# Kernel tuning notes

Hardware: AMD Instinct MI355X
Metric: run time of the kernel (lower is better)

Reference implementation:

```python
import jax, jax.numpy as jnp
import numpy as np
from jax import lax

N, D, H = 4096, 768, 16384


def setup_inputs() -> dict:
    key = jax.random.key(0)
    k0, k1, k2, k3, k4, k5, k6 = jax.random.split(key, 7)
    bound_e = 1.0 / np.sqrt(D)   # kaiming_uniform(a=sqrt(5)) on (H, D) -> bound 1/sqrt(fan_in)
    bound_d = 1.0 / np.sqrt(H)   # nn.Linear default init, fan_in = H
    return {
        "vision_embeddings": jax.random.normal(k0, (N, D), dtype=jnp.float32),
        "text_embeddings": jax.random.normal(k1, (N, D), dtype=jnp.float32),
        "encoder": jax.random.uniform(k2, (H, D), jnp.float32, -bound_e, bound_e),
        "Wv": jax.random.uniform(k3, (D, H), jnp.float32, -bound_d, bound_d),
        "bv": jax.random.uniform(k4, (D,), jnp.float32, -bound_d, bound_d),
        "Wt": jax.random.uniform(k5, (D, H), jnp.float32, -bound_d, bound_d),
        "bt": jax.random.uniform(k6, (D,), jnp.float32, -bound_d, bound_d),
        "topk": 32,
    }


def _l2norm(x, axis):
    return x / jnp.maximum(jnp.linalg.norm(x, axis=axis, keepdims=True), 1e-12)


def _encode(emb, encoder, topk):
    # F.normalize rows, then cdist(p=2) between unit vectors: ||a-b|| = sqrt(2-2 a.b)
    w = _l2norm(encoder, axis=1)            # [H, D]
    e = _l2norm(emb, axis=1)                # [N, D]
    cos = jnp.einsum("nd,hd->nh", e, w)     # [N, H]
    dist = jnp.sqrt(jnp.maximum(2.0 - 2.0 * cos, 0.0))
    sim = 2.0 - dist                         # [N, H]
    # kthvalue(abs, k=H-topk) == (topk+1)-th largest; keep strictly-greater entries
    abs_f = jnp.abs(sim)
    thres = lax.top_k(abs_f, topk + 1)[0][:, -1]  # [N]
    mask = (abs_f > thres[:, None]).astype(sim.dtype)
    return sim * mask


def reference(vision_embeddings, text_embeddings, encoder, Wv, bv, Wt, bt, topk):
    latent_v = _encode(vision_embeddings, encoder, topk)          # [N, H]
    recon_v = jnp.einsum("nh,dh->nd", latent_v, Wv) + bv          # [N, D]
    latent_t = _encode(text_embeddings, encoder, topk)            # [N, H]
    recon_t = jnp.einsum("nh,dh->nd", latent_t, Wt) + bt          # [N, D]
    return (recon_v, recon_t, latent_v, latent_t)
```

## Files before the change

kernel.cpp:

```cpp
#include <hip/hip_runtime.h>
#include <math.h>


#define N_ROWS 4096
#define D_DIM  768
#define H_DIM  16384
#define M_TOT  8192
#define TOPK   32
#define MARGIN 1e-3f
#define SEL_CAP 40
#define AMB_CAP 64
#define CAP2   512

typedef __attribute__((ext_vector_type(8))) short short8;
typedef __attribute__((ext_vector_type(4))) float floatx4;

__device__ inline unsigned short bf16_rne(float f) {
    unsigned u = __float_as_uint(f);
    unsigned r = u + 0x7fffu + ((u >> 16) & 1u);
    return (unsigned short)(r >> 16);
}

__device__ inline void gload16(const unsigned short* g, unsigned short* l) {
    __builtin_amdgcn_global_load_lds(
        (const __attribute__((address_space(1))) void*)g,
        (__attribute__((address_space(3))) void*)l, 16, 0, 0);
}

__global__ void split_all_kernel(const float* __restrict__ embv,
                                 const float* __restrict__ embt,
                                 const float* __restrict__ enc,
                                 unsigned short* __restrict__ Ahi,
                                 unsigned short* __restrict__ Alo,
                                 unsigned short* __restrict__ Bh,
                                 float* __restrict__ invA,
                                 float* __restrict__ invB)
{
    int row = blockIdx.x;
    int tid = threadIdx.x;
    const float* src;
    unsigned short *hi, *lo;
    float* invp;
    if (row < N_ROWS) {
        src = embv + (size_t)row * D_DIM;
        hi = Ahi + (size_t)row * D_DIM; lo = Alo + (size_t)row * D_DIM;
        invp = invA + row;
    } else if (row < 2 * N_ROWS) {
        int r = row - N_ROWS;
        src = embt + (size_t)r * D_DIM;
        hi = Ahi + (size_t)row * D_DIM; lo = Alo + (size_t)row * D_DIM;
        invp = invA + row;
    } else {
        int r = row - 2 * N_ROWS;
        src = enc + (size_t)r * D_DIM;
        hi = Bh + (size_t)r * D_DIM; lo = nullptr;
        invp = invB + r;
    }
    __shared__ float red[4];
    const float4* s4 = reinterpret_cast<const float4*>(src);
    float4 v = make_float4(0.f, 0.f, 0.f, 0.f);
    float ss = 0.f;
    if (tid < 192) {
        v = s4[tid];
        ss = v.x * v.x + v.y * v.y + v.z * v.z + v.w * v.w;
    }
    #pragma unroll
    for (int o = 32; o > 0; o >>= 1) ss += __shfl_down(ss, o);
    int wave = tid >> 6, lane = tid & 63;
    if (lane == 0) red[wave] = ss;
    __syncthreads();
    if (tid == 0) {
        float tot = red[0] + red[1] + red[2];
        red[0] = 1.f / fmaxf(sqrtf(tot), 1e-12f);
    }
    __syncthreads();
    float inv = red[0];
    if (tid == 0) *invp = inv;
    if (tid < 192) {
        float x[4] = {v.x * inv, v.y * inv, v.z * inv, v.w * inv};
        unsigned short hh[4], ll[4];
        #pragma unroll
        for (int t = 0; t < 4; t++) {
            hh[t] = bf16_rne(x[t]);
            float hf = __uint_as_float((unsigned)hh[t] << 16);
            ll[t] = bf16_rne(x[t] - hf);
        }
        ushort4 h4; h4.x = hh[0]; h4.y = hh[1]; h4.z = hh[2]; h4.w = hh[3];
        *reinterpret_cast<ushort4*>(hi + tid * 4) = h4;
        if (lo) {
            ushort4 l4; l4.x = ll[0]; l4.y = ll[1]; l4.z = ll[2]; l4.w = ll[3];
            *reinterpret_cast<ushort4*>(lo + tid * 4) = l4;
        }
    }
}

#define GBK 32

__global__ __launch_bounds__(256, 4)
void gemm_mfma_kernel(const unsigned short* __restrict__ Ahi,
                      const unsigned short* __restrict__ Alo,
                      const unsigned short* __restrict__ Bh,
                      float* __restrict__ latent)
{
    __shared__ unsigned short sA[2][128 * GBK];
    __shared__ unsigned short sB[128 * GBK];

    int tid = threadIdx.x;
    int lane = tid & 63;
    int wave = tid >> 6;
    int wr = (wave >> 1) * 64;
    int wc = (wave & 1) * 64;
    int m = lane & 15;
    int q = lane >> 4;

    int row0 = blockIdx.y * 128;
    int col0 = blockIdx.x * 128;

    int p0 = tid, p1 = tid + 256;
    int r0 = ((p0 >> 5) << 3) | (p0 & 7), q0 = (p0 >> 3) & 3;
    int r1 = ((p1 >> 5) << 3) | (p1 & 7), q1 = (p1 >> 3) & 3;
    size_t aoff0 = (size_t)(row0 + r0) * D_DIM + q0 * 8;
    size_t aoff1 = (size_t)(row0 + r1) * D_DIM + q1 * 8;
    size_t boff0 = (size_t)(col0 + r0) * D_DIM + q0 * 8;
    size_t boff1 = (size_t)(col0 + r1) * D_DIM + q1 * 8;

    int am0 = wr + m;
    int bn0 = wc + m;
    int offA = ((am0 >> 3) << 8) + (q << 6) + ((am0 & 7) << 3);
    int offB = ((bn0 >> 3) << 8) + (q << 6) + ((bn0 & 7) << 3);

    floatx4 acc[4][4];
    #pragma unroll
    for (int i = 0; i < 4; i++)
        #pragma unroll
        for (int j = 0; j < 4; j++)
            acc[i][j] = (floatx4){0.f, 0.f, 0.f, 0.f};

    for (int k0 = 0; k0 < D_DIM; k0 += GBK) {
        gload16(Ahi + aoff0 + k0, &sA[0][p0 * 8]);
        gload16(Ahi + aoff1 + k0, &sA[0][p1 * 8]);
        gload16(Alo + aoff0 + k0, &sA[1][p0 * 8]);
        gload16(Alo + aoff1 + k0, &sA[1][p1 * 8]);
        gload16(Bh + boff0 + k0, &sB[p0 * 8]);
        gload16(Bh + boff1 + k0, &sB[p1 * 8]);
        __syncthreads();

        short8 fah[4], fal[4];
        #pragma unroll
        for (int i = 0; i < 4; i++) {
            fah[i] = *(const short8*)&sA[0][offA + i * 512];
            fal[i] = *(const short8*)&sA[1][offA + i * 512];
        }
        #pragma unroll
        for (int j = 0; j < 4; j++) {
            short8 fb = *(const short8*)&sB[offB + j * 512];
            #pragma unroll
            for (int i = 0; i < 4; i++) {
                acc[i][j] = __builtin_amdgcn_mfma_f32_16x16x32_bf16(fah[i], fb, acc[i][j], 0, 0, 0);
                acc[i][j] = __builtin_amdgcn_mfma_f32_16x16x32_bf16(fal[i], fb, acc[i][j], 0, 0, 0);
            }
        }
        __syncthreads();
    }

    #pragma unroll
    for (int i = 0; i < 4; i++) {
        #pragma unroll
        for (int r = 0; r < 4; r++) {
            int grow = row0 + wr + i * 16 + q * 4 + r;
            float* dst = latent + (size_t)grow * H_DIM + col0 + wc + m;
            #pragma unroll
            for (int j = 0; j < 4; j++) {
                float cosv = acc[i][j][r];
                float sim = 2.f - sqrtf(fmaxf(2.f - 2.f * cosv, 0.f));
                dst[j * 16] = sim;
            }
        }
    }
}

__global__ __launch_bounds__(256)
void select_kernel(float* __restrict__ latent,
                   int* __restrict__ sel_cnt,
                   int* __restrict__ sel_idx,
                   float* __restrict__ sel_val,
                   int* __restrict__ amb_cnt,
                   int* __restrict__ amb_idx)
{
    int row = blockIdx.x;
    int tid = threadIdx.x;
    float* v = latent + (size_t)row * H_DIM;
    const float4* v4 = (const float4*)v;
    float4* vw = (float4*)v;

    __shared__ _Float16 hbuf[H_DIM];
    __shared__ float smax[256];
    __shared__ float sca[CAP2];
    __shared__ int   sci[CAP2];
    __shared__ float sT;
    __shared__ int scnt, svstar, skept, samb;

    float mx = -1.f;
    #pragma unroll 4
    for (int k = 0; k < 16; k++) {
        int i = tid + 256 * k;
        float4 x = v4[i];
        float a0 = fabsf(x.x), a1 = fabsf(x.y), a2 = fabsf(x.z), a3 = fabsf(x.w);
        hbuf[4 * i + 0] = (_Float16)a0;
        hbuf[4 * i + 1] = (_Float16)a1;
        hbuf[4 * i + 2] = (_Float16)a2;
        hbuf[4 * i + 3] = (_Float16)a3;
        mx = fmaxf(mx, fmaxf(fmaxf(a0, a1), fmaxf(a2, a3)));
    }
    smax[tid] = mx;
    if (tid == 0) { scnt = 0; svstar = 0x7FFFFFFF; skept = 0; samb = 0; }
    __syncthreads();

    int gt = 0;
    for (int j = 0; j < 256; j++) {
        float mj = smax[j];
        gt += (mj > mx || (mj == mx && j < tid)) ? 1 : 0;
    }
    if (gt == 32) sT = mx;
    __syncthreads();
    float Tm = sT - MARGIN;

    #pragma unroll 4
    for (int k = 0; k < 16; k++) {
        int i = tid + 256 * k;
        float a[4];
        a[0] = (float)hbuf[4 * i + 0]; a[1] = (float)hbuf[4 * i + 1];
        a[2] = (float)hbuf[4 * i + 2]; a[3] = (float)hbuf[4 * i + 3];
        bool any = (a[0] >= Tm) | (a[1] >= Tm) | (a[2] >= Tm) | (a[3] >= Tm);
        if (any) {
            #pragma unroll
            for (int t = 0; t < 4; t++) {
                if (a[t] >= Tm) {
                    int c = atomicAdd(&scnt, 1);
                    if (c < CAP2) { sci[c] = 4 * i + t; sca[c] = v[4 * i + t]; }
                }
            }
        }
        vw[i] = make_float4(0.f, 0.f, 0.f, 0.f);
    }
    __syncthreads();

    int C = min(scnt, CAP2);
    for (int c = tid; c < C; c += 256) {
        float a = fabsf(sca[c]);
        int g = 0;
        for (int j = 0; j < C; j++) {
            float aj = fabsf(sca[j]);
            g += (aj > a || (aj == a && j < c)) ? 1 : 0;
        }
        if (g <= TOPK) atomicMin(&svstar, __float_as_int(a));
    }
    __syncthreads();
    float vs = __int_as_float(svstar);

    for (int c = tid; c < C; c += 256) {
        float f = sca[c];
        float a = fabsf(f);
        int idx = sci[c];
        if (a > vs + MARGIN) {
            int s = atomicAdd(&skept, 1);
            sel_idx[(size_t)row * SEL_CAP + s] = idx;
            sel_val[(size_t)row * SEL_CAP + s] = f;
            v[idx] = f;
        } else if (a >= vs - MARGIN) {
            int s = atomicAdd(&samb, 1);
            if (s < AMB_CAP) amb_idx[(size_t)row * AMB_CAP + s] = idx;
        }
    }
    __syncthreads();
    if (tid == 0) { sel_cnt[row] = skept; amb_cnt[row] = min(samb, AMB_CAP); }
}

__global__ void refine_kernel(const float* __restrict__ embv,
                              const float* __restrict__ embt,
                              const float* __restrict__ enc,
                              const float* __restrict__ invA,
                              const float* __restrict__ invB,
                              float* __restrict__ latent,
                              int* __restrict__ sel_cnt,
                              int* __restrict__ sel_idx,
                              float* __restrict__ sel_val,
                              const int* __restrict__ amb_cnt,
                              const int* __restrict__ amb_idx)
{
    int row = blockIdx.x;
    int s = amb_cnt[row];
    if (s == 0) return;
    int tid = threadIdx.x;
    int m = sel_cnt[row];
    int need = TOPK - m;
    float* v = latent + (size_t)row * H_DIM;
    if (need <= 0) return;
    __shared__ float ex[AMB_CAP];
    __shared__ int evs, kc;
    const float* src = (row < N_ROWS) ? embv + (size_t)row * D_DIM
                                      : embt + (size_t)(row - N_ROWS) * D_DIM;
    float ia = invA[row];
    int wave = tid >> 6, lane = tid & 63;
    for (int a = wave; a < s; a += 4) {
        int h = amb_idx[(size_t)row * AMB_CAP + a];
        const float* w = enc + (size_t)h * D_DIM;
        float d = 0.f;
        for (int t = lane; t < D_DIM; t += 64) d += src[t] * w[t];
        #pragma unroll
        for (int o = 32; o > 0; o >>= 1) d += __shfl_down(d, o);
        if (lane == 0) {
            float cosv = d * ia * invB[h];
            ex[a] = 2.f - sqrtf(fmaxf(2.f - 2.f * cosv, 0.f));
        }
    }
    if (tid == 0) { evs = 0x7FFFFFFF; kc = 0; }
    __syncthreads();
    if (tid < s) {
        float mya = fabsf(ex[tid]);
        int g = 0;
        for (int j = 0; j < s; j++) {
            float aj = fabsf(ex[j]);
            g += (aj > mya || (aj == mya && j < tid)) ? 1 : 0;
        }
        if (g <= need) atomicMin(&evs, __float_as_int(mya));
    }
    __syncthreads();
    float ep = __int_as_float(evs);
    if (tid < s) {
        int idx = amb_idx[(size_t)row * AMB_CAP + tid];
        float e = ex[tid];
        if (fabsf(e) > ep) {
            int sl = atomicAdd(&kc, 1);
            v[idx] = e;
            sel_idx[(size_t)row * SEL_CAP + m + sl] = idx;
            sel_val[(size_t)row * SEL_CAP + m + sl] = e;
        }
    }
    __syncthreads();
    if (tid == 0) sel_cnt[row] = m + kc;
}

__global__ void transpose_kernel(const float* __restrict__ Wv,
                                 const float* __restrict__ Wt,
                                 float* __restrict__ WvT,
                                 float* __restrict__ WtT)
{
    int z = blockIdx.z;
    const float* W = z ? Wt : Wv;
    float* WT = z ? WtT : WvT;
    __shared__ float tile[32][33];
    int tx = threadIdx.x & 31;
    int ty = threadIdx.x >> 5;
    int h0 = blockIdx.x * 32;
    int d0 = blockIdx.y * 32;
    #pragma unroll
    for (int t = 0; t < 4; t++)
        tile[ty + t * 8][tx] = W[(size_t)(d0 + ty + t * 8) * H_DIM + h0 + tx];
    __syncthreads();
    #pragma unroll
    for (int t = 0; t < 4; t++)
        WT[(size_t)(h0 + ty + t * 8) * D_DIM + d0 + tx] = tile[tx][ty + t * 8];
}

__global__ void recon_kernel(const float* __restrict__ Wv_,
                             const float* __restrict__ Wt_,
                             const float* __restrict__ bv,
                             const float* __restrict__ bt,
                             const int* __restrict__ sel_cnt,
                             const int* __restrict__ sel_idx,
                             const float* __restrict__ sel_val,
                             long sh, long sd,
                             float* __restrict__ out)
{
    int n = blockIdx.x;
    int z = blockIdx.y;
    int row = z * N_ROWS + n;
    const float* W = z ? Wt_ : Wv_;
    const float* bias = z ? bt : bv;
    float* o = out + (size_t)z * N_ROWS * D_DIM + (size_t)n * D_DIM;

    __shared__ int s_idx[SEL_CAP];
    __shared__ float s_val[SEL_CAP];
    __shared__ int s_cnt;
    int tid = threadIdx.x;
    if (tid == 0) s_cnt = sel_cnt[row];
    __syncthreads();
    int cnt = s_cnt;
    if (tid < cnt) {
        s_idx[tid] = sel_idx[(size_t)row * SEL_CAP + tid];
        s_val[tid] = sel_val[(size_t)row * SEL_CAP + tid];
    }
    __syncthreads();

    for (int d = tid; d < D_DIM; d += 256) {
        float acc = bias[d];
        for (int j = 0; j < cnt; j++)
            acc += s_val[j] * W[(size_t)s_idx[j] * sh + (size_t)d * sd];
        o[d] = acc;
    }
}

__global__ void row_invnorm_kernel(const float* __restrict__ x,
                                   float* __restrict__ inv, int rows) {
    int row = blockIdx.x * 4 + (threadIdx.x >> 6);
    int lane = threadIdx.x & 63;
    if (row >= rows) return;
    const float4* p = reinterpret_cast<const float4*>(x + (size_t)row * D_DIM);
    float ss = 0.f;
    #pragma unroll
    for (int i = 0; i < 3; i++) {
        float4 v = p[lane + i * 64];
        ss += v.x * v.x + v.y * v.y + v.z * v.z + v.w * v.w;
    }
    #pragma unroll
    for (int off = 32; off > 0; off >>= 1) ss += __shfl_down(ss, off);
    if (lane == 0) inv[row] = 1.f / fmaxf(sqrtf(ss), 1e-12f);
}

#define BM 128
#define BN 128
#define BK 16
__global__ __launch_bounds__(256)
void gemm_sim_kernel(const float* __restrict__ embv,
                     const float* __restrict__ embt,
                     const float* __restrict__ enc,
                     const float* __restrict__ inv_emb,
                     const float* __restrict__ inv_enc,
                     float* __restrict__ latent)
{
    int z = blockIdx.z;
    const float* A = z ? embt : embv;
    const float* invA = inv_emb + z * N_ROWS;
    float* C = latent + (size_t)z * N_ROWS * H_DIM;
    __shared__ float As[BK][BM + 4];
    __shared__ float Bs[BK][BN + 4];
    int tid = threadIdx.x;
    int tx = tid & 15, ty = tid >> 4;
    int row0 = blockIdx.y * BM, col0 = blockIdx.x * BN;
    float acc[8][8];
    #pragma unroll
    for (int i = 0; i < 8; i++)
        #pragma unroll
        for (int j = 0; j < 8; j++) acc[i][j] = 0.f;
    for (int k0 = 0; k0 < D_DIM; k0 += BK) {
        #pragma unroll
        for (int t = 0; t < 2; t++) {
            int idx = t * 256 + tid;
            int r = idx >> 2, c4 = idx & 3;
            float4 va = *reinterpret_cast<const float4*>(
                A + (size_t)(row0 + r) * D_DIM + k0 + c4 * 4);
            As[c4 * 4 + 0][r] = va.x; As[c4 * 4 + 1][r] = va.y;
            As[c4 * 4 + 2][r] = va.z; As[c4 * 4 + 3][r] = va.w;
            float4 vb = *reinterpret_cast<const float4*>(
                enc + (size_t)(col0 + r) * D_DIM + k0 + c4 * 4);
            Bs[c4 * 4 + 0][r] = vb.x; Bs[c4 * 4 + 1][r] = vb.y;
            Bs[c4 * 4 + 2][r] = vb.z; Bs[c4 * 4 + 3][r] = vb.w;
        }
        __syncthreads();
        #pragma unroll
        for (int kk = 0; kk < BK; kk++) {
            float a[8], b[8];
            *reinterpret_cast<float4*>(&a[0]) = *reinterpret_cast<const float4*>(&As[kk][ty * 8]);
            *reinterpret_cast<float4*>(&a[4]) = *reinterpret_cast<const float4*>(&As[kk][ty * 8 + 4]);
            *reinterpret_cast<float4*>(&b[0]) = *reinterpret_cast<const float4*>(&Bs[kk][tx * 8]);
            *reinterpret_cast<float4*>(&b[4]) = *reinterpret_cast<const float4*>(&Bs[kk][tx * 8 + 4]);
            #pragma unroll
            for (int i = 0; i < 8; i++)
                #pragma unroll
                for (int j = 0; j < 8; j++)
                    acc[i][j] = fmaf(a[i], b[j], acc[i][j]);
        }
        __syncthreads();
    }
    #pragma unroll
    for (int i = 0; i < 8; i++) {
        int n = row0 + ty * 8 + i;
        float sa = invA[n];
        float* Crow = C + (size_t)n * H_DIM + col0 + tx * 8;
        float tmp[8];
        #pragma unroll
        for (int j = 0; j < 8; j++) {
            float cosv = acc[i][j] * sa * inv_enc[col0 + tx * 8 + j];
            tmp[j] = 2.f - sqrtf(fmaxf(2.f - 2.f * cosv, 0.f));
        }
        float4 o0 = {tmp[0], tmp[1], tmp[2], tmp[3]};
        float4 o1 = {tmp[4], tmp[5], tmp[6], tmp[7]};
        *reinterpret_cast<float4*>(Crow) = o0;
        *reinterpret_cast<float4*>(Crow + 4) = o1;
    }
}

__global__ void legacy_select_kernel(float* __restrict__ latent,
                                     const int* __restrict__ topk_p,
                                     int* __restrict__ sel_cnt,
                                     int* __restrict__ sel_idx,
                                     float* __restrict__ sel_val)
{
    int row = blockIdx.x;
    float* v = latent + (size_t)row * H_DIM;
    int tid = threadIdx.x;
    __shared__ unsigned hist[256];
    __shared__ unsigned s_prefix;
    __shared__ int s_k;
    __shared__ int s_cnt;
    int k = topk_p[0] + 1;
    unsigned prefix = 0;
    for (int shift = 24; shift >= 0; shift -= 8) {
        hist[tid] = 0;
        __syncthreads();
        unsigned pmask = (shift == 24) ? 0u : (0xFFFFFFFFu << (shift + 8));
        for (int i = tid; i < H_DIM; i += 256) {
            unsigned u = __float_as_uint(v[i]) & 0x7FFFFFFFu;
            if ((u & pmask) == prefix)
                atomicAdd(&hist[(u >> shift) & 255u], 1u);
        }
        __syncthreads();
        if (tid == 0) {
            int c = 0, b = 255;
            for (; b >= 0; b--) {
                c += (int)hist[b];
                if (c >= k) break;
            }
            if (b < 0) b = 0;
            s_prefix = prefix | ((unsigned)b << shift);
            s_k = k - (c - (int)hist[b]);
        }
        __syncthreads();
        prefix = s_prefix;
        k = s_k;
        __syncthreads();
    }
    float thres = __uint_as_float(prefix);
    if (tid == 0) s_cnt = 0;
    __syncthreads();
    for (int i = tid; i < H_DIM; i += 256) {
        float x = v[i];
        bool keep = (fabsf(x) > thres);
        v[i] = keep ? x : 0.f;
        if (keep) {
            int slot = atomicAdd(&s_cnt, 1);
            if (slot < SEL_CAP) {
                sel_idx[(size_t)row * SEL_CAP + slot] = i;
                sel_val[(size_t)row * SEL_CAP + slot] = x;
            }
        }
    }
    __syncthreads();
    if (tid == 0) sel_cnt[row] = (s_cnt > SEL_CAP) ? SEL_CAP : s_cnt;
}

extern "C" void kernel_launch(void* const* d_in, const int* in_sizes, int n_in,
                              void* d_out, int out_size, void* d_ws, size_t ws_size,
                              hipStream_t stream) {
    const float* embv = (const float*)d_in[0];
    const float* embt = (const float*)d_in[1];
    const float* enc  = (const float*)d_in[2];
    const float* Wv   = (const float*)d_in[3];
    const float* bv   = (const float*)d_in[4];
    const float* Wt   = (const float*)d_in[5];
    const float* bt   = (const float*)d_in[6];
    const int* topk   = (const int*)d_in[7];
    float* out = (float*)d_out;

    float* recon_out = out;
    float* latent = out + (size_t)2 * N_ROWS * D_DIM;

    char* ws = (char*)d_ws;
    size_t off = 0;
    float* invA = (float*)(ws + off);            off += (size_t)M_TOT * 4;
    float* invB = (float*)(ws + off);            off += (size_t)H_DIM * 4;
    int*   sel_cnt = (int*)(ws + off);           off += (size_t)M_TOT * 4;
    int*   amb_cnt = (int*)(ws + off);           off += (size_t)M_TOT * 4;
    int*   sel_idx = (int*)(ws + off);           off += (size_t)M_TOT * SEL_CAP * 4;
    float* sel_val = (float*)(ws + off);         off += (size_t)M_TOT * SEL_CAP * 4;
    int*   amb_idx = (int*)(ws + off);           off += (size_t)M_TOT * AMB_CAP * 4;
    unsigned short* Ahi = (unsigned short*)(ws + off); off += (size_t)M_TOT * D_DIM * 2;
    unsigned short* Alo = (unsigned short*)(ws + off); off += (size_t)M_TOT * D_DIM * 2;
    unsigned short* Bh  = (unsigned short*)(ws + off); off += (size_t)H_DIM * D_DIM * 2;
    size_t core_need = off;
    float* WvT = (float*)(ws + off);
    float* WtT = WvT + (size_t)D_DIM * H_DIM;
    size_t full_need = off + (size_t)2 * D_DIM * H_DIM * 4;

    if (ws_size >= core_need) {
        bool use_T = ws_size >= full_need;

        split_all_kernel<<<2 * N_ROWS + H_DIM, 256, 0, stream>>>(
            embv, embt, enc, Ahi, Alo, Bh, invA, invB);

        gemm_mfma_kernel<<<dim3(H_DIM / 128, M_TOT / 128), 256, 0, stream>>>(
            Ahi, Alo, Bh, latent);

        select_kernel<<<M_TOT, 256, 0, stream>>>(latent,
            sel_cnt, sel_idx, sel_val, amb_cnt, amb_idx);

        refine_kernel<<<M_TOT, 256, 0, stream>>>(embv, embt, enc, invA, invB,
            latent, sel_cnt, sel_idx, sel_val, amb_cnt, amb_idx);

        if (use_T) {
            transpose_kernel<<<dim3(H_DIM / 32, D_DIM / 32, 2), 256, 0, stream>>>(
                Wv, Wt, WvT, WtT);
            recon_kernel<<<dim3(N_ROWS, 2), 256, 0, stream>>>(
                WvT, WtT, bv, bt, sel_cnt, sel_idx, sel_val, (long)D_DIM, 1L, recon_out);
        } else {
            recon_kernel<<<dim3(N_ROWS, 2), 256, 0, stream>>>(
                Wv, Wt, bv, bt, sel_cnt, sel_idx, sel_val, 1L, (long)H_DIM, recon_out);
        }
    } else {
        size_t o2 = 0;
        float* inv_enc = (float*)(ws + o2); o2 += (size_t)H_DIM * 4;
        float* inv_emb = (float*)(ws + o2); o2 += (size_t)2 * N_ROWS * 4;
        int*   l_cnt = (int*)(ws + o2);     o2 += (size_t)2 * N_ROWS * 4;
        int*   l_idx = (int*)(ws + o2);     o2 += (size_t)2 * N_ROWS * SEL_CAP * 4;
        float* l_val = (float*)(ws + o2);   o2 += (size_t)2 * N_ROWS * SEL_CAP * 4;
        row_invnorm_kernel<<<H_DIM / 4, 256, 0, stream>>>(enc, inv_enc, H_DIM);
        row_invnorm_kernel<<<N_ROWS / 4, 256, 0, stream>>>(embv, inv_emb, N_ROWS);
        row_invnorm_kernel<<<N_ROWS / 4, 256, 0, stream>>>(embt, inv_emb + N_ROWS, N_ROWS);
        dim3 g(H_DIM / BN, N_ROWS / BM, 2);
        gemm_sim_kernel<<<g, 256, 0, stream>>>(embv, embt, enc, inv_emb, inv_enc, latent);
        legacy_select_kernel<<<2 * N_ROWS, 256, 0, stream>>>(latent, topk, l_cnt, l_idx, l_val);
        recon_kernel<<<dim3(N_ROWS, 2), 256, 0, stream>>>(
            Wv, Wt, bv, bt, l_cnt, l_idx, l_val, 1L, (long)H_DIM, recon_out);
    }
}
```

Measured before the change: 1.723 ms.

## Double-buffer GEMM LDS tiles, swizzle workgroups, use nontemporal latent stores

```diff
diff --git a/kernel.cpp b/kernel.cpp
--- a/kernel.cpp
+++ b/kernel.cpp
@@ -95,15 +95,16 @@
 }
 
 #define GBK 32
-
-__global__ __launch_bounds__(256, 4)
+#define NTILE (D_DIM / GBK)
+
+__global__ __launch_bounds__(256, 3)
 void gemm_mfma_kernel(const unsigned short* __restrict__ Ahi,
                       const unsigned short* __restrict__ Alo,
                       const unsigned short* __restrict__ Bh,
                       float* __restrict__ latent)
 {
-    __shared__ unsigned short sA[2][128 * GBK];
-    __shared__ unsigned short sB[128 * GBK];
+    __shared__ unsigned short sA[2][2][128 * GBK];
+    __shared__ unsigned short sB[2][128 * GBK];
 
     int tid = threadIdx.x;
     int lane = tid & 63;
@@ -113,8 +114,15 @@
     int m = lane & 15;
     int q = lane >> 4;
 
-    int row0 = blockIdx.y * 128;
-    int col0 = blockIdx.x * 128;
+    unsigned nwgx = gridDim.x;
+    unsigned lid = blockIdx.y * nwgx + blockIdx.x;
+    unsigned cpx = (nwgx * gridDim.y) >> 3;
+    unsigned swz = (lid & 7u) * cpx + (lid >> 3);
+    int bx = (int)(swz % nwgx);
+    int by = (int)(swz / nwgx);
+
+    int row0 = by * 128;
+    int col0 = bx * 128;
 
     int p0 = tid, p1 = tid + 256;
     int r0 = ((p0 >> 5) << 3) | (p0 & 7), q0 = (p0 >> 3) & 3;
@@ -136,32 +144,54 @@
         for (int j = 0; j < 4; j++)
             acc[i][j] = (floatx4){0.f, 0.f, 0.f, 0.f};
 
-    for (int k0 = 0; k0 < D_DIM; k0 += GBK) {
-        gload16(Ahi + aoff0 + k0, &sA[0][p0 * 8]);
-        gload16(Ahi + aoff1 + k0, &sA[0][p1 * 8]);
-        gload16(Alo + aoff0 + k0, &sA[1][p0 * 8]);
-        gload16(Alo + aoff1 + k0, &sA[1][p1 * 8]);
-        gload16(Bh + boff0 + k0, &sB[p0 * 8]);
-        gload16(Bh + boff1 + k0, &sB[p1 * 8]);
-        __syncthreads();
-
-        short8 fah[4], fal[4];
+    auto stage = [&](int t, int b) {
+        int k0 = t * GBK;
+        gload16(Ahi + aoff0 + k0, &sA[b][0][p0 * 8]);
+        gload16(Ahi + aoff1 + k0, &sA[b][0][p1 * 8]);
+        gload16(Alo + aoff0 + k0, &sA[b][1][p0 * 8]);
+        gload16(Alo + aoff1 + k0, &sA[b][1][p1 * 8]);
+        gload16(Bh + boff0 + k0, &sB[b][p0 * 8]);
+        gload16(Bh + boff1 + k0, &sB[b][p1 * 8]);
+    };
+
+    auto compute = [&](int b) {
+        short8 fah[4], fal[4], fbv[4];
         #pragma unroll
         for (int i = 0; i < 4; i++) {
-            fah[i] = *(const short8*)&sA[0][offA + i * 512];
-            fal[i] = *(const short8*)&sA[1][offA + i * 512];
-        }
+            fah[i] = *(const short8*)&sA[b][0][offA + i * 512];
+            fal[i] = *(const short8*)&sA[b][1][offA + i * 512];
+        }
+        #pragma unroll
+        for (int j = 0; j < 4; j++)
+            fbv[j] = *(const short8*)&sB[b][offB + j * 512];
+        __builtin_amdgcn_s_setprio(1);
         #pragma unroll
         for (int j = 0; j < 4; j++) {
-            short8 fb = *(const short8*)&sB[offB + j * 512];
             #pragma unroll
             for (int i = 0; i < 4; i++) {
-                acc[i][j] = __builtin_amdgcn_mfma_f32_16x16x32_bf16(fah[i], fb, acc[i][j], 0, 0, 0);
-                acc[i][j] = __builtin_amdgcn_mfma_f32_16x16x32_bf16(fal[i], fb, acc[i][j], 0, 0, 0);
+                acc[i][j] = __builtin_amdgcn_mfma_f32_16x16x32_bf16(fah[i], fbv[j], acc[i][j], 0, 0, 0);
+                acc[i][j] = __builtin_amdgcn_mfma_f32_16x16x32_bf16(fal[i], fbv[j], acc[i][j], 0, 0, 0);
             }
         }
-        __syncthreads();
-    }
+        __builtin_amdgcn_s_setprio(0);
+    };
+
+    stage(0, 0);
+    int cur = 0;
+    for (int t = 0; t < NTILE - 1; ++t) {
+        stage(t + 1, cur ^ 1);
+        asm volatile("s_waitcnt vmcnt(6)" ::: "memory");
+        __builtin_amdgcn_s_barrier();
+        __builtin_amdgcn_sched_barrier(0);
+        compute(cur);
+        __builtin_amdgcn_sched_barrier(0);
+        __builtin_amdgcn_s_barrier();
+        cur ^= 1;
+    }
+    asm volatile("s_waitcnt vmcnt(0)" ::: "memory");
+    __builtin_amdgcn_s_barrier();
+    __builtin_amdgcn_sched_barrier(0);
+    compute(cur);
 
     #pragma unroll
     for (int i = 0; i < 4; i++) {
@@ -173,7 +203,7 @@
             for (int j = 0; j < 4; j++) {
                 float cosv = acc[i][j][r];
                 float sim = 2.f - sqrtf(fmaxf(2.f - 2.f * cosv, 0.f));
-                dst[j * 16] = sim;
+                __builtin_nontemporal_store(sim, dst + j * 16);
             }
         }
     }
@@ -190,8 +220,8 @@
     int row = blockIdx.x;
     int tid = threadIdx.x;
     float* v = latent + (size_t)row * H_DIM;
-    const float4* v4 = (const float4*)v;
-    float4* vw = (float4*)v;
+    const floatx4* v4 = (const floatx4*)v;
+    floatx4* vw = (floatx4*)v;
 
     __shared__ _Float16 hbuf[H_DIM];
     __shared__ float smax[256];
@@ -204,7 +234,7 @@
     #pragma unroll 4
     for (int k = 0; k < 16; k++) {
         int i = tid + 256 * k;
-        float4 x = v4[i];
+        floatx4 x = __builtin_nontemporal_load(&v4[i]);
         float a0 = fabsf(x.x), a1 = fabsf(x.y), a2 = fabsf(x.z), a3 = fabsf(x.w);
         hbuf[4 * i + 0] = (_Float16)a0;
         hbuf[4 * i + 1] = (_Float16)a1;
@@ -241,7 +271,8 @@
                 }
             }
         }
-        vw[i] = make_float4(0.f, 0.f, 0.f, 0.f);
+        floatx4 zz = (floatx4){0.f, 0.f, 0.f, 0.f};
+        __builtin_nontemporal_store(zz, &vw[i]);
     }
     __syncthreads();
 
```

Result: faster. 1.583 ms (-8.1%).
